# Kernel optimization log

Measured on AMD Instinct MI355X. Metric: run time of the kernel, lower is better.

Reference implementation:

```python
import jax, jax.numpy as jnp
import numpy as np

B, N, M, D = 8, 4096, 4096, 128


def _cdist(x, y):
    # Euclidean distance via gram trick (matches torch.cdist p=2 math)
    # x: (B,N,D), y: (B,M,D) -> (B,N,M)
    x2 = jnp.sum(x * x, axis=-1)  # (B,N)
    y2 = jnp.sum(y * y, axis=-1)  # (B,M)
    xy = jnp.einsum('bnd,bmd->bnm', x, y)  # (B,N,M)
    sq = x2[:, :, None] + y2[:, None, :] - 2.0 * xy
    return jnp.sqrt(jnp.maximum(sq, 0.0))


def setup_inputs() -> dict:
    key = jax.random.key(0)
    k1, k2 = jax.random.split(key)
    predicted_set = jax.random.normal(k1, (B, N, D), dtype=jnp.float32)
    target_set = jax.random.normal(k2, (B, M, D), dtype=jnp.float32)
    return {"predicted_set": predicted_set, "target_set": target_set}


def reference(predicted_set, target_set):
    pairwise = _cdist(predicted_set, target_set)       # (B,N,M)
    forward_distance = jnp.min(pairwise, axis=1)        # (B,M)  (min over predicted points)
    backward_distance = jnp.min(pairwise, axis=0)       # (N,M)  (min over BATCH, as in original code)
    # reduction = 'mean'
    return jnp.mean(forward_distance) + jnp.mean(backward_distance)
```

## Files before the change

kernel.cpp:

```cpp
#include <hip/hip_runtime.h>
#include <hip/hip_fp8.h>

#define BB 8
#define NN 4096
#define MM 4096
#define DD 128

typedef float f32x4 __attribute__((ext_vector_type(4)));
typedef long  long2v __attribute__((ext_vector_type(2)));


__global__ __launch_bounds__(256)
void prep_all(const float* __restrict__ x, const float* __restrict__ y,
              unsigned char* __restrict__ xq, unsigned char* __restrict__ yq,
              float* __restrict__ x2, float* __restrict__ y2,
              unsigned int* __restrict__ fwd, float* __restrict__ bsum,
              float* __restrict__ fsum, unsigned int* __restrict__ counter) {
    int gtid = blockIdx.x * blockDim.x + threadIdx.x;
    if (gtid < BB * MM) fwd[gtid] = 0x7f800000u;
    if (gtid == 0) { *bsum = 0.0f; *fsum = 0.0f; *counter = 0u; }

    int row = gtid >> 5;
    int k4  = gtid & 31;
    const float* src;
    unsigned char* dst;
    float* sq;
    if (row < BB * NN) {
        src = x; dst = xq; sq = x2;
    } else {
        src = y; dst = yq; sq = y2; row -= BB * NN;
    }
    f32x4 v = ((const f32x4*)src)[(size_t)row * 32 + k4];
    float s = v.x * v.x + v.y * v.y + v.z * v.z + v.w * v.w;
    unsigned int p32;
    p32  = (unsigned int)__hip_cvt_float_to_fp8(v.x, __HIP_SATFINITE, __HIP_E4M3);
    p32 |= (unsigned int)__hip_cvt_float_to_fp8(v.y, __HIP_SATFINITE, __HIP_E4M3) << 8;
    p32 |= (unsigned int)__hip_cvt_float_to_fp8(v.z, __HIP_SATFINITE, __HIP_E4M3) << 16;
    p32 |= (unsigned int)__hip_cvt_float_to_fp8(v.w, __HIP_SATFINITE, __HIP_E4M3) << 24;

    int k    = k4 << 2;
    int kk   = k >> 5;
    int h    = kk >> 1;
    int p    = kk & 1;
    int quad = (k >> 3) & 3;
    size_t dstoff = ((size_t)(row >> 4) * 2 + h) * 1024
                  + (size_t)(quad * 16 + (row & 15)) * 16 + p * 8 + (k & 7);
    *(unsigned int*)(dst + dstoff) = p32;

    #pragma unroll
    for (int m = 16; m; m >>= 1) s += __shfl_xor(s, m, 64);
    if (k4 == 0) sq[row] = s;
}

__global__ __launch_bounds__(256, 4)
void chamfer_main(const unsigned char* __restrict__ xq, const unsigned char* __restrict__ yq,
                  const float* __restrict__ x2, const float* __restrict__ y2,
                  unsigned int* __restrict__ fwd, float* __restrict__ bpart) {
    __shared__ float x2s[BB][128];
    __shared__ float y2s[BB][32];
    __shared__ unsigned int fbuf[BB][32];
    __shared__ float red[4];

    const int tid  = threadIdx.x;
    const int lane = tid & 63;
    const int wave = tid >> 6;
    const int quad = lane >> 4;
    const int l15  = lane & 15;

    const int id  = blockIdx.x;
    const int xcd = id & 7;
    const int j   = id >> 3;
    const int nb  = j & 31;
    const int mb  = xcd * 16 + (j >> 5);
    const int n0b = nb * 128;
    const int n0w = n0b + wave * 32;
    const int m0  = mb * 32;

    const size_t lane16 = (size_t)lane * 16;
    const unsigned char* xbase = xq + (size_t)(n0w >> 4) * 2048 + lane16;
    const unsigned char* ybase = yq + (size_t)(m0 >> 4) * 2048 + lane16;

    for (int i = tid; i < BB * 128; i += 256)
        x2s[i >> 7][i & 127] = x2[(size_t)(i >> 7) * NN + n0b + (i & 127)];
    if (tid < BB * 32) {
        y2s[tid >> 5][tid & 31] = y2[(size_t)(tid >> 5) * MM + m0 + (tid & 31)];
        ((unsigned int*)fbuf)[tid] = 0x7f800000u;
    }
    __syncthreads();

    long2v fx[2][2][2], fy[2][2][2];
    auto loadb = [&](int b, int s) {
        const unsigned char* xb = xbase + ((size_t)b << 19);
        const unsigned char* yb = ybase + ((size_t)b << 19);
        #pragma unroll
        for (int g2 = 0; g2 < 2; ++g2)
            #pragma unroll
            for (int h = 0; h < 2; ++h) {
                fx[s][g2][h] = *(const long2v*)(xb + ((g2 * 2 + h) << 10));
                fy[s][g2][h] = *(const long2v*)(yb + ((g2 * 2 + h) << 10));
            }
    };
    loadb(0, 0);

    const float INF = __builtin_inff();
    f32x4 bmin[2][2];
    #pragma unroll
    for (int fi = 0; fi < 2; ++fi)
        #pragma unroll
        for (int fj = 0; fj < 2; ++fj)
            bmin[fi][fj] = (f32x4){INF, INF, INF, INF};

    #pragma unroll 2
    for (int b = 0; b < BB; ++b) {
        const int cur = b & 1;
        if (b < BB - 1) loadb(b + 1, cur ^ 1);

        f32x4 acc[2][2];
        #pragma unroll
        for (int fi = 0; fi < 2; ++fi)
            #pragma unroll
            for (int fj = 0; fj < 2; ++fj)
                acc[fi][fj] = (f32x4){0.f, 0.f, 0.f, 0.f};

        #pragma unroll
        for (int h = 0; h < 2; ++h)
            #pragma unroll
            for (int p = 0; p < 2; ++p)
                #pragma unroll
                for (int fi = 0; fi < 2; ++fi)
                    #pragma unroll
                    for (int fj = 0; fj < 2; ++fj)
                        acc[fi][fj] = __builtin_amdgcn_mfma_f32_16x16x32_fp8_fp8(
                            fx[cur][fi][h][p], fy[cur][fj][h][p], acc[fi][fj], 0, 0, 0);

        float y2v[2];
        y2v[0] = y2s[b][l15];
        y2v[1] = y2s[b][16 + l15];
        float fm[2] = {INF, INF};
        #pragma unroll
        for (int fi = 0; fi < 2; ++fi) {
            const f32x4 x2v = *(const f32x4*)&x2s[b][wave * 32 + fi * 16 + quad * 4];
            #pragma unroll
            for (int fj = 0; fj < 2; ++fj)
                #pragma unroll
                for (int e = 0; e < 4; ++e) {
                    float sqv = fmaf(-2.0f, acc[fi][fj][e], x2v[e] + y2v[fj]);
                    bmin[fi][fj][e] = fminf(bmin[fi][fj][e], sqv);
                    fm[fj]          = fminf(fm[fj], sqv);
                }
        }
        #pragma unroll
        for (int fj = 0; fj < 2; ++fj) {
            atomicMin(&fbuf[b][fj * 16 + l15],
                      __float_as_uint(fmaxf(fm[fj], 0.0f)));
        }
    }
    __syncthreads();

    {
        int b = tid >> 5, c = tid & 31;
        atomicMin(&fwd[(size_t)b * MM + m0 + c], fbuf[b][c]);
    }

    float s = 0.0f;
    #pragma unroll
    for (int fi = 0; fi < 2; ++fi)
        #pragma unroll
        for (int fj = 0; fj < 2; ++fj)
            #pragma unroll
            for (int e = 0; e < 4; ++e)
                s += sqrtf(fmaxf(bmin[fi][fj][e], 0.0f));
    #pragma unroll
    for (int off = 32; off; off >>= 1) s += __shfl_down(s, off, 64);
    if (lane == 0) red[wave] = s;
    __syncthreads();
    if (tid == 0) bpart[id] = red[0] + red[1] + red[2] + red[3];
}

__global__ __launch_bounds__(256)
void finalize_kernel(const unsigned int* __restrict__ fwd,
                     const float* __restrict__ bpart,
                     float* __restrict__ bsum, float* __restrict__ fsum,
                     unsigned int* __restrict__ counter, float* __restrict__ out) {
    __shared__ float redf[4], redb[4];
    __shared__ int isLast;
    const int tid = threadIdx.x, lane = tid & 63, wave = tid >> 6;
    const int gtid = blockIdx.x * 256 + tid;
    uint4 u = ((const uint4*)fwd)[gtid];
    float sf = sqrtf(__uint_as_float(u.x)) + sqrtf(__uint_as_float(u.y)) +
               sqrtf(__uint_as_float(u.z)) + sqrtf(__uint_as_float(u.w));
    float sb = (gtid < 4096) ? bpart[gtid] : 0.0f;
    #pragma unroll
    for (int off = 32; off; off >>= 1) {
        sf += __shfl_down(sf, off, 64);
        sb += __shfl_down(sb, off, 64);
    }
    if (lane == 0) { redf[wave] = sf; redb[wave] = sb; }
    __syncthreads();
    if (tid == 0) {
        atomicAdd(fsum, redf[0] + redf[1] + redf[2] + redf[3]);
        atomicAdd(bsum, redb[0] + redb[1] + redb[2] + redb[3]);
        __threadfence();
        unsigned int c = atomicAdd(counter, 1u);
        isLast = (c == gridDim.x - 1) ? 1 : 0;
        if (isLast) {
            __threadfence();
            float fs = __hip_atomic_load(fsum, __ATOMIC_RELAXED,
                                         __HIP_MEMORY_SCOPE_AGENT);
            float bs = __hip_atomic_load(bsum, __ATOMIC_RELAXED,
                                         __HIP_MEMORY_SCOPE_AGENT);
            out[0] = fs / (float)(BB * MM) + bs / ((float)NN * (float)MM);
        }
    }
}

extern "C" void kernel_launch(void* const* d_in, const int* in_sizes, int n_in,
                              void* d_out, int out_size, void* d_ws, size_t ws_size,
                              hipStream_t stream) {
    const float* x = (const float*)d_in[0];
    const float* y = (const float*)d_in[1];
    float* out = (float*)d_out;

    char* w = (char*)d_ws;
    unsigned char* xq = (unsigned char*)(w);
    unsigned char* yq = (unsigned char*)(w + 4194304);
    float*    x2 = (float*)(w + 8388608);
    float*    y2 = (float*)(w + 8519680);
    unsigned int* fwd = (unsigned int*)(w + 8650752);
    float*    bpart = (float*)(w + 8781824);
    float*    bsum = (float*)(w + 8798208);
    float*    fsum = (float*)(w + 8798212);
    unsigned int* counter = (unsigned int*)(w + 8798216);

    prep_all<<<(2 * BB * NN * 32) / 256, 256, 0, stream>>>(x, y, xq, yq, x2, y2,
                                                           fwd, bsum, fsum, counter);
    chamfer_main<<<4096, 256, 0, stream>>>(xq, yq, x2, y2, fwd, bpart);
    finalize_kernel<<<32, 256, 0, stream>>>(fwd, bpart, bsum, fsum, counter, out);
}
```

Measured before the change: 123.8 us.

## Fuse finalize into main kernel via last-block reduction and packed fp8 conversion

Removes the separate finalize kernel launch. The last block of chamfer_main, found through an atomic counter, now reduces the forward minima and the backward partials itself. The fp8 quantisation in prep switches to the packed cvt_pk_fp8_f32 builtin, and a sched_barrier is placed after the next-batch prefetch to pin instruction scheduling. This saves one launch, but the final reduction now runs serially in a single block and every block pays a threadfence.

```diff
diff --git a/kernel.cpp b/kernel.cpp
--- a/kernel.cpp
+++ b/kernel.cpp
@@ -14,11 +14,10 @@
 void prep_all(const float* __restrict__ x, const float* __restrict__ y,
               unsigned char* __restrict__ xq, unsigned char* __restrict__ yq,
               float* __restrict__ x2, float* __restrict__ y2,
-              unsigned int* __restrict__ fwd, float* __restrict__ bsum,
-              float* __restrict__ fsum, unsigned int* __restrict__ counter) {
+              unsigned int* __restrict__ fwd, unsigned int* __restrict__ counter) {
     int gtid = blockIdx.x * blockDim.x + threadIdx.x;
     if (gtid < BB * MM) fwd[gtid] = 0x7f800000u;
-    if (gtid == 0) { *bsum = 0.0f; *fsum = 0.0f; *counter = 0u; }
+    if (gtid == 0) *counter = 0u;
 
     int row = gtid >> 5;
     int k4  = gtid & 31;
@@ -32,11 +31,8 @@
     }
     f32x4 v = ((const f32x4*)src)[(size_t)row * 32 + k4];
     float s = v.x * v.x + v.y * v.y + v.z * v.z + v.w * v.w;
-    unsigned int p32;
-    p32  = (unsigned int)__hip_cvt_float_to_fp8(v.x, __HIP_SATFINITE, __HIP_E4M3);
-    p32 |= (unsigned int)__hip_cvt_float_to_fp8(v.y, __HIP_SATFINITE, __HIP_E4M3) << 8;
-    p32 |= (unsigned int)__hip_cvt_float_to_fp8(v.z, __HIP_SATFINITE, __HIP_E4M3) << 16;
-    p32 |= (unsigned int)__hip_cvt_float_to_fp8(v.w, __HIP_SATFINITE, __HIP_E4M3) << 24;
+    unsigned int p32 = (unsigned int)__builtin_amdgcn_cvt_pk_fp8_f32(v.x, v.y, 0, false);
+    p32 = (unsigned int)__builtin_amdgcn_cvt_pk_fp8_f32(v.z, v.w, (int)p32, true);
 
     int k    = k4 << 2;
     int kk   = k >> 5;
@@ -55,11 +51,13 @@
 __global__ __launch_bounds__(256, 4)
 void chamfer_main(const unsigned char* __restrict__ xq, const unsigned char* __restrict__ yq,
                   const float* __restrict__ x2, const float* __restrict__ y2,
-                  unsigned int* __restrict__ fwd, float* __restrict__ bpart) {
+                  unsigned int* __restrict__ fwd, float* __restrict__ bpart,
+                  unsigned int* __restrict__ counter, float* __restrict__ out) {
     __shared__ float x2s[BB][128];
     __shared__ float y2s[BB][32];
     __shared__ unsigned int fbuf[BB][32];
-    __shared__ float red[4];
+    __shared__ float red[4], redb[4];
+    __shared__ int isLast;
 
     const int tid  = threadIdx.x;
     const int lane = tid & 63;
@@ -114,6 +112,7 @@
     for (int b = 0; b < BB; ++b) {
         const int cur = b & 1;
         if (b < BB - 1) loadb(b + 1, cur ^ 1);
+        __builtin_amdgcn_sched_barrier(0);
 
         f32x4 acc[2][2];
         #pragma unroll
@@ -175,41 +174,35 @@
     if (lane == 0) red[wave] = s;
     __syncthreads();
     if (tid == 0) bpart[id] = red[0] + red[1] + red[2] + red[3];
-}
-
-__global__ __launch_bounds__(256)
-void finalize_kernel(const unsigned int* __restrict__ fwd,
-                     const float* __restrict__ bpart,
-                     float* __restrict__ bsum, float* __restrict__ fsum,
-                     unsigned int* __restrict__ counter, float* __restrict__ out) {
-    __shared__ float redf[4], redb[4];
-    __shared__ int isLast;
-    const int tid = threadIdx.x, lane = tid & 63, wave = tid >> 6;
-    const int gtid = blockIdx.x * 256 + tid;
-    uint4 u = ((const uint4*)fwd)[gtid];
-    float sf = sqrtf(__uint_as_float(u.x)) + sqrtf(__uint_as_float(u.y)) +
-               sqrtf(__uint_as_float(u.z)) + sqrtf(__uint_as_float(u.w));
-    float sb = (gtid < 4096) ? bpart[gtid] : 0.0f;
-    #pragma unroll
-    for (int off = 32; off; off >>= 1) {
-        sf += __shfl_down(sf, off, 64);
-        sb += __shfl_down(sb, off, 64);
-    }
-    if (lane == 0) { redf[wave] = sf; redb[wave] = sb; }
+
+    __threadfence();
     __syncthreads();
     if (tid == 0) {
-        atomicAdd(fsum, redf[0] + redf[1] + redf[2] + redf[3]);
-        atomicAdd(bsum, redb[0] + redb[1] + redb[2] + redb[3]);
+        unsigned int c = atomicAdd(counter, 1u);
+        isLast = (c == (unsigned int)(gridDim.x - 1)) ? 1 : 0;
+    }
+    __syncthreads();
+    if (isLast) {
         __threadfence();
-        unsigned int c = atomicAdd(counter, 1u);
-        isLast = (c == gridDim.x - 1) ? 1 : 0;
-        if (isLast) {
-            __threadfence();
-            float fs = __hip_atomic_load(fsum, __ATOMIC_RELAXED,
-                                         __HIP_MEMORY_SCOPE_AGENT);
-            float bs = __hip_atomic_load(bsum, __ATOMIC_RELAXED,
-                                         __HIP_MEMORY_SCOPE_AGENT);
-            out[0] = fs / (float)(BB * MM) + bs / ((float)NN * (float)MM);
+        float sf = 0.0f, sb = 0.0f;
+        const uint4* fw4 = (const uint4*)fwd;
+        for (int i = tid; i < (BB * MM) / 4; i += 256) {
+            uint4 u = fw4[i];
+            sf += sqrtf(__uint_as_float(u.x)) + sqrtf(__uint_as_float(u.y)) +
+                  sqrtf(__uint_as_float(u.z)) + sqrtf(__uint_as_float(u.w));
+        }
+        for (int i = tid; i < 4096; i += 256) sb += bpart[i];
+        #pragma unroll
+        for (int off = 32; off; off >>= 1) {
+            sf += __shfl_down(sf, off, 64);
+            sb += __shfl_down(sb, off, 64);
+        }
+        if (lane == 0) { red[wave] = sf; redb[wave] = sb; }
+        __syncthreads();
+        if (tid == 0) {
+            float ftot = red[0] + red[1] + red[2] + red[3];
+            float btot = redb[0] + redb[1] + redb[2] + redb[3];
+            out[0] = ftot / (float)(BB * MM) + btot / ((float)NN * (float)MM);
         }
     }
 }
@@ -228,12 +221,9 @@
     float*    y2 = (float*)(w + 8519680);
     unsigned int* fwd = (unsigned int*)(w + 8650752);
     float*    bpart = (float*)(w + 8781824);
-    float*    bsum = (float*)(w + 8798208);
-    float*    fsum = (float*)(w + 8798212);
-    unsigned int* counter = (unsigned int*)(w + 8798216);
+    unsigned int* counter = (unsigned int*)(w + 8798208);
 
     prep_all<<<(2 * BB * NN * 32) / 256, 256, 0, stream>>>(x, y, xq, yq, x2, y2,
-                                                           fwd, bsum, fsum, counter);
-    chamfer_main<<<4096, 256, 0, stream>>>(xq, yq, x2, y2, fwd, bpart);
-    finalize_kernel<<<32, 256, 0, stream>>>(fwd, bpart, bsum, fsum, counter, out);
+                                                           fwd, counter);
+    chamfer_main<<<4096, 256, 0, stream>>>(xq, yq, x2, y2, fwd, bpart, counter, out);
 }
```

Result: slower. 469.5 us (+279.2%).
